# Kernel optimization log

Measured on AMD Instinct MI355X. Metric: run time of the kernel, lower is better.

The kernel has to match this reference:

```python
import jax, jax.numpy as jnp
import numpy as np

EPS = 1e-5
LOSS_WEIGHT = 0.3
IGNORE_INDEX = -100


def rmsnorm(x, w):
    # x: (B,S,D), w: (D,)
    var = jnp.mean(x * x, axis=-1, keepdims=True)
    return x * jax.lax.rsqrt(var + EPS) * w


def cross_entropy(logits, targets):
    # logits: (B,T,V), targets: (B,T) int; ignore_index=-100, mean reduction
    logp = jax.nn.log_softmax(logits, axis=-1)
    valid = targets != IGNORE_INDEX
    safe_t = jnp.where(valid, targets, 0)
    nll = -jnp.take_along_axis(logp, safe_t[..., None], axis=-1)[..., 0]
    nll = jnp.where(valid, nll, 0.0)
    return jnp.sum(nll) / jnp.maximum(jnp.sum(valid), 1)


def setup_inputs() -> dict:
    key = jax.random.key(0)
    ks = jax.random.split(key, 5)
    B, S, D, V, H = 1, 2048, 1024, 50257, 3
    hidden = jax.random.normal(ks[0], (B, S, D), dtype=jnp.float32)
    targets = jax.random.randint(ks[1], (B, S), 0, V, dtype=jnp.int64)
    emb_w = jax.random.normal(ks[2], (V, D), dtype=jnp.float32) * 0.02
    main_norm_w = jnp.ones((D,), dtype=jnp.float32)
    aux_proj_w = jax.random.normal(ks[3], (H - 1, D, D), dtype=jnp.float32) * 0.02
    aux_norm_w = jnp.ones((H - 1, D), dtype=jnp.float32)
    aux_out_w = jax.random.normal(ks[4], (H - 1, V, D), dtype=jnp.float32) * 0.02
    return {"hidden": hidden, "targets": targets, "emb_w": emb_w,
            "main_norm_w": main_norm_w, "aux_proj_w": aux_proj_w,
            "aux_norm_w": aux_norm_w, "aux_out_w": aux_out_w}


def reference(hidden, targets, emb_w, main_norm_w, aux_proj_w, aux_norm_w, aux_out_w):
    # Main head: norm -> tied vocab projection
    main_logits = jnp.einsum('bsd,vd->bsv', rmsnorm(hidden, main_norm_w), emb_w)
    main_loss = cross_entropy(main_logits[:, :-1, :], targets[:, 1:])

    # Auxiliary heads predict t+2, t+3, ...
    n_aux = aux_proj_w.shape[0]
    aux_losses = []
    for i in range(n_aux):
        k = i + 2
        h = jnp.einsum('bsd,ed->bse', hidden, aux_proj_w[i])  # d_model -> d_model
        logits = jnp.einsum('bsd,vd->bsv', rmsnorm(h, aux_norm_w[i]), aux_out_w[i])
        aux_losses.append(cross_entropy(logits[:, :-k, :], targets[:, k:]))
    total_aux = sum(aux_losses) / len(aux_losses) if aux_losses else jnp.float32(0.0)
    loss = main_loss + LOSS_WEIGHT * total_aux
    return main_logits, loss
```

## Files before the change

### kernel.cpp

```cpp
#include <hip/hip_runtime.h>
#include <hip/hip_bf16.h>


typedef __hip_bfloat16 bf16;
typedef __attribute__((ext_vector_type(8))) short bf16x8;
typedef __attribute__((ext_vector_type(4))) float f32x4;

typedef const __attribute__((address_space(1))) void* gptr_t;
typedef __attribute__((address_space(3))) void* lptr_t;

#define S_LEN   2048
#define DMODEL  1024
#define VOCAB   50257
#define NPADR   50304
#define NT128   393
#define NBLK    6288

__device__ __forceinline__ void gload_lds16(const void* g, void* l) {
  __builtin_amdgcn_global_load_lds((gptr_t)g, (lptr_t)l, 16, 0, 0);
}

__global__ __launch_bounds__(256) void k_cvt(const float* __restrict__ src,
                                             bf16* __restrict__ dst,
                                             long rows_src, long rows_pad) {
  const long total4 = rows_pad << 8;
  for (long i = (long)blockIdx.x * 256 + threadIdx.x; i < total4;
       i += (long)gridDim.x * 256) {
    const long e = i << 2;
    const long row = e >> 10;
    alignas(8) bf16 o[4];
    if (row < rows_src) {
      const float4 v = *(const float4*)(src + e);
      o[0] = __float2bfloat16(v.x); o[1] = __float2bfloat16(v.y);
      o[2] = __float2bfloat16(v.z); o[3] = __float2bfloat16(v.w);
    } else {
      o[0] = o[1] = o[2] = o[3] = __float2bfloat16(0.f);
    }
    *(uint2*)(dst + e) = *(const uint2*)o;
  }
}

__global__ __launch_bounds__(256) void k_rms(const float* __restrict__ x,
                                             const float* __restrict__ w,
                                             bf16* __restrict__ xn) {
  const int row = blockIdx.x;
  const int t = threadIdx.x;
  const float4 v = ((const float4*)(x + (size_t)row * DMODEL))[t];
  float ss = v.x*v.x + v.y*v.y + v.z*v.z + v.w*v.w;
  #pragma unroll
  for (int d = 1; d < 64; d <<= 1) ss += __shfl_xor(ss, d, 64);
  __shared__ float red[4];
  if ((t & 63) == 0) red[t >> 6] = ss;
  __syncthreads();
  const float tot = red[0] + red[1] + red[2] + red[3];
  const float scale = rsqrtf(tot * (1.f / DMODEL) + 1e-5f);
  const float4 wv = ((const float4*)w)[t];
  alignas(8) bf16 o[4];
  o[0] = __float2bfloat16(v.x * scale * wv.x);
  o[1] = __float2bfloat16(v.y * scale * wv.y);
  o[2] = __float2bfloat16(v.z * scale * wv.z);
  o[3] = __float2bfloat16(v.w * scale * wv.w);
  *(uint2*)(xn + (size_t)row * DMODEL + t * 4) = *(const uint2*)o;
}

template<bool WRITE_OUT>
__global__ __launch_bounds__(256, 2)
void k_gemm128(const bf16* __restrict__ A, const bf16* __restrict__ B,
               float* __restrict__ C, long ldc, int Nvalid,
               const int* __restrict__ targets, int shift,
               float* __restrict__ pmax, float* __restrict__ psum,
               float* __restrict__ ptgt, int ntiles) {
  __shared__ bf16 As[2][128 * 32];
  __shared__ bf16 Bs[2][128 * 32];
  __shared__ float lds_m[128][2];
  __shared__ float lds_s[128][2];
  __shared__ int lds_tgt[128];

  const int t = threadIdx.x;
  const int w = t >> 6, l = t & 63, g = l >> 4, q = l & 15;
  const int wr = w >> 1, wc = w & 1;
  const int id = blockIdx.x;
  int bm, bn;
  if (id < 6272) {
    const int x = id & 7, u = id >> 3;
    bm = u & 15;
    bn = x * 49 + (u >> 4);
  } else {
    bm = id - 6272;
    bn = 392;
  }

  f32x4 acc[4][4];
  #pragma unroll
  for (int i = 0; i < 4; ++i)
    #pragma unroll
    for (int j = 0; j < 4; ++j)
      #pragma unroll
      for (int r = 0; r < 4; ++r) acc[i][j][r] = 0.f;

  char* dA = (char*)As + w * 1024;
  char* dB = (char*)Bs + w * 1024;
  const int scol = ((t & 3) * 16) ^ (((t >> 5) & 1) * 32);
  const char* gA0 = (const char*)(A + (size_t)(bm * 128 + (t >> 2)) * DMODEL) + scol;
  const char* gA1 = gA0 + (size_t)64 * DMODEL * 2;
  const char* gB0 = (const char*)(B + (size_t)(bn * 128 + (t >> 2)) * DMODEL) + scol;
  const char* gB1 = gB0 + (size_t)64 * DMODEL * 2;

  const int laneoff = (q * 64 + g * 16) ^ (((q >> 3) & 1) << 5);
  const char* rdA = (const char*)As + wr * 4096 + laneoff;
  const char* rdB = (const char*)Bs + wc * 4096 + laneoff;

  for (int k0 = 0; k0 < 16; ++k0) {
    const int kb = k0 * 128;
    gload_lds16(gA0 + kb, dA);
    gload_lds16(gA1 + kb, dA + 4096);
    gload_lds16(gA0 + kb + 64, dA + 8192);
    gload_lds16(gA1 + kb + 64, dA + 12288);
    gload_lds16(gB0 + kb, dB);
    gload_lds16(gB1 + kb, dB + 4096);
    gload_lds16(gB0 + kb + 64, dB + 8192);
    gload_lds16(gB1 + kb + 64, dB + 12288);
    __syncthreads();
    bf16x8 a[4], b[4];
    #pragma unroll
    for (int mi = 0; mi < 4; ++mi) a[mi] = *(const bf16x8*)(rdA + mi * 1024);
    #pragma unroll
    for (int ni = 0; ni < 4; ++ni) b[ni] = *(const bf16x8*)(rdB + ni * 1024);
    __builtin_amdgcn_s_setprio(1);
    #pragma unroll
    for (int mi = 0; mi < 4; ++mi)
      #pragma unroll
      for (int ni = 0; ni < 4; ++ni)
        acc[mi][ni] = __builtin_amdgcn_mfma_f32_16x16x32_bf16(a[mi], b[ni], acc[mi][ni], 0, 0, 0);
    __builtin_amdgcn_s_setprio(0);
    #pragma unroll
    for (int mi = 0; mi < 4; ++mi) a[mi] = *(const bf16x8*)(rdA + 8192 + mi * 1024);
    #pragma unroll
    for (int ni = 0; ni < 4; ++ni) b[ni] = *(const bf16x8*)(rdB + 8192 + ni * 1024);
    __builtin_amdgcn_s_setprio(1);
    #pragma unroll
    for (int mi = 0; mi < 4; ++mi)
      #pragma unroll
      for (int ni = 0; ni < 4; ++ni)
        acc[mi][ni] = __builtin_amdgcn_mfma_f32_16x16x32_bf16(a[mi], b[ni], acc[mi][ni], 0, 0, 0);
    __builtin_amdgcn_s_setprio(0);
    __syncthreads();
  }

  if constexpr (WRITE_OUT) {
    #pragma unroll
    for (int mi = 0; mi < 4; ++mi) {
      #pragma unroll
      for (int r = 0; r < 4; ++r) {
        const long row = bm * 128 + wr * 64 + mi * 16 + g * 4 + r;
        #pragma unroll
        for (int ni = 0; ni < 4; ++ni) {
          const int col = bn * 128 + wc * 64 + ni * 16 + q;
          if (col < Nvalid)
            __builtin_nontemporal_store(acc[mi][ni][r], &C[row * ldc + col]);
        }
      }
    }
  }

  if (t < 128) {
    const int rowg = bm * 128 + t;
    lds_tgt[t] = (rowg < S_LEN - shift) ? targets[rowg + shift] : -1;
  }
  __syncthreads();
  #pragma unroll
  for (int mi = 0; mi < 4; ++mi) {
    #pragma unroll
    for (int r = 0; r < 4; ++r) {
      const int rl = wr * 64 + mi * 16 + g * 4 + r;
      const int tgt = lds_tgt[rl];
      float v[4];
      #pragma unroll
      for (int ni = 0; ni < 4; ++ni) {
        const int n = bn * 128 + wc * 64 + ni * 16 + q;
        const float av = acc[mi][ni][r];
        if (n == tgt) ptgt[bm * 128 + rl] = av;
        v[ni] = (n < Nvalid) ? av : -1e30f;
      }
      float m = fmaxf(fmaxf(v[0], v[1]), fmaxf(v[2], v[3]));
      #pragma unroll
      for (int d = 1; d < 16; d <<= 1) m = fmaxf(m, __shfl_xor(m, d, 64));
      float s = 0.f;
      #pragma unroll
      for (int ni = 0; ni < 4; ++ni) s += __expf(v[ni] - m);
      #pragma unroll
      for (int d = 1; d < 16; d <<= 1) s += __shfl_xor(s, d, 64);
      if (q == 0) { lds_m[rl][wc] = m; lds_s[rl][wc] = s; }
    }
  }
  __syncthreads();
  if (t < 128) {
    const float m0 = lds_m[t][0], m1 = lds_m[t][1];
    const float s0 = lds_s[t][0], s1 = lds_s[t][1];
    const float M = fmaxf(m0, m1);
    const float Ssum = s0 * __expf(m0 - M) + s1 * __expf(m1 - M);
    const size_t idx = (size_t)(bm * 128 + t) * ntiles + bn;
    pmax[idx] = M;
    psum[idx] = Ssum;
  }
}

__global__ __launch_bounds__(256, 2)
void k_gemm(const bf16* __restrict__ A, const bf16* __restrict__ B,
            float* __restrict__ C, long ldc, int Nvalid) {
  constexpr int K = DMODEL;
  __shared__ bf16 As[128 * 32];
  __shared__ bf16 Bs[128 * 32];

  const int t = threadIdx.x;
  const int bn = blockIdx.x, bm = blockIdx.y;
  const int w = t >> 6, l = t & 63, g = l >> 4, q = l & 15;
  const int wr = w >> 1, wc = w & 1;

  f32x4 acc[4][4];
  #pragma unroll
  for (int i = 0; i < 4; ++i)
    #pragma unroll
    for (int j = 0; j < 4; ++j)
      #pragma unroll
      for (int r = 0; r < 4; ++r) acc[i][j][r] = 0.f;

  char* lA0 = (char*)As + w * 1024;
  char* lA1 = (char*)As + 4096 + w * 1024;
  char* lB0 = (char*)Bs + w * 1024;
  char* lB1 = (char*)Bs + 4096 + w * 1024;
  const char* gA0 = (const char*)(A + (size_t)(bm * 128 + (t >> 2)) * K) + (t & 3) * 16;
  const char* gA1 = gA0 + (size_t)64 * K * 2;
  const char* gB0 = (const char*)(B + (size_t)(bn * 128 + (t >> 2)) * K) + (t & 3) * 16;
  const char* gB1 = gB0 + (size_t)64 * K * 2;

  for (int k0 = 0; k0 < K; k0 += 32) {
    const int kb = k0 * 2;
    gload_lds16(gA0 + kb, lA0);
    gload_lds16(gA1 + kb, lA1);
    gload_lds16(gB0 + kb, lB0);
    gload_lds16(gB1 + kb, lB1);
    __syncthreads();
    bf16x8 a[4], b[4];
    #pragma unroll
    for (int mi = 0; mi < 4; ++mi)
      a[mi] = *(const bf16x8*)&As[(wr * 64 + mi * 16 + q) * 32 + g * 8];
    #pragma unroll
    for (int ni = 0; ni < 4; ++ni)
      b[ni] = *(const bf16x8*)&Bs[(wc * 64 + ni * 16 + q) * 32 + g * 8];
    #pragma unroll
    for (int mi = 0; mi < 4; ++mi)
      #pragma unroll
      for (int ni = 0; ni < 4; ++ni)
        acc[mi][ni] = __builtin_amdgcn_mfma_f32_16x16x32_bf16(a[mi], b[ni], acc[mi][ni], 0, 0, 0);
    __syncthreads();
  }

  #pragma unroll
  for (int mi = 0; mi < 4; ++mi) {
    #pragma unroll
    for (int r = 0; r < 4; ++r) {
      const long row = bm * 128 + wr * 64 + mi * 16 + g * 4 + r;
      #pragma unroll
      for (int ni = 0; ni < 4; ++ni) {
        const int col = bn * 128 + wc * 64 + ni * 16 + q;
        if (col < Nvalid) C[row * ldc + col] = acc[mi][ni][r];
      }
    }
  }
}

__global__ __launch_bounds__(64) void k_combine(const float* __restrict__ pmax,
                                                const float* __restrict__ psum,
                                                const float* __restrict__ ptgt,
                                                float* __restrict__ nll,
                                                int ntiles, int nv) {
  const int r = blockIdx.x;
  const int l = threadIdx.x;
  float M = -1e30f, Ssum = 0.f;
  for (int tl = l; tl < ntiles; tl += 64) {
    const float m = pmax[(size_t)r * ntiles + tl];
    const float s = psum[(size_t)r * ntiles + tl];
    const float nM = fmaxf(M, m);
    Ssum = Ssum * __expf(M - nM) + s * __expf(m - nM);
    M = nM;
  }
  #pragma unroll
  for (int d = 1; d < 64; d <<= 1) {
    const float m2 = __shfl_xor(M, d, 64);
    const float s2 = __shfl_xor(Ssum, d, 64);
    const float nM = fmaxf(M, m2);
    Ssum = Ssum * __expf(M - nM) + s2 * __expf(m2 - nM);
    M = nM;
  }
  if (l == 0) nll[r] = (r < nv) ? (M + logf(Ssum) - ptgt[r]) : 0.f;
}

__global__ __launch_bounds__(256) void k_loss(const float* __restrict__ nll,
                                              float* __restrict__ out) {
  __shared__ float sh[256];
  const int t = threadIdx.x;
  float sums[3];
  #pragma unroll
  for (int h = 0; h < 3; ++h) {
    const int nv = 2047 - h;
    float s = 0.f;
    for (int r = t; r < nv; r += 256) s += nll[h * 2048 + r];
    sh[t] = s; __syncthreads();
    for (int off = 128; off > 0; off >>= 1) {
      if (t < off) sh[t] += sh[t + off];
      __syncthreads();
    }
    sums[h] = sh[0]; __syncthreads();
  }
  if (t == 0)
    out[0] = sums[0] / 2047.f + 0.3f * 0.5f * (sums[1] / 2046.f + sums[2] / 2045.f);
}

extern "C" void kernel_launch(void* const* d_in, const int* in_sizes, int n_in,
                              void* d_out, int out_size, void* d_ws, size_t ws_size,
                              hipStream_t stream) {
  const float* hidden      = (const float*)d_in[0];
  const int*   targets     = (const int*)d_in[1];
  const float* emb_w       = (const float*)d_in[2];
  const float* main_norm_w = (const float*)d_in[3];
  const float* aux_proj_w  = (const float*)d_in[4];
  const float* aux_norm_w  = (const float*)d_in[5];
  const float* aux_out_w   = (const float*)d_in[6];
  float* out = (float*)d_out;

  char* ws = (char*)d_ws;
  bf16*  Wb    = (bf16*)(ws);
  bf16*  hb    = (bf16*)(ws + 104857600);
  bf16*  xn    = (bf16*)(ws + 109051904);
  bf16*  projb = (bf16*)(ws + 113246208);
  float* hbuf  = (float*)(ws + 117440512);
  float* pmax  = (float*)(ws + 125829120);
  float* psum  = (float*)(ws + 129105920);
  float* ptgt  = (float*)(ws + 132382720);
  float* nll   = (float*)(ws + 132390912);

  k_cvt<<<2048, 256, 0, stream>>>(hidden, hb, 2048, 2048);
  k_cvt<<<2048, 256, 0, stream>>>(aux_proj_w, projb, 2048, 2048);
  k_rms<<<2048, 256, 0, stream>>>(hidden, main_norm_w, xn);

  k_cvt<<<2048, 256, 0, stream>>>(emb_w, Wb, VOCAB, NPADR);
  k_gemm128<true><<<NBLK, 256, 0, stream>>>(
      xn, Wb, out, VOCAB, VOCAB, targets, 1, pmax, psum, ptgt, NT128);
  k_combine<<<2048, 64, 0, stream>>>(pmax, psum, ptgt, nll, NT128, 2047);

  for (int i = 0; i < 2; ++i) {
    k_cvt<<<2048, 256, 0, stream>>>(aux_out_w + (size_t)i * VOCAB * DMODEL, Wb, VOCAB, NPADR);
    k_gemm<<<dim3(8, 16), 256, 0, stream>>>(
        hb, projb + (size_t)i * DMODEL * DMODEL, hbuf, DMODEL, DMODEL);
    k_rms<<<2048, 256, 0, stream>>>(hbuf, aux_norm_w + (size_t)i * DMODEL, xn);
    k_gemm128<false><<<NBLK, 256, 0, stream>>>(
        xn, Wb, nullptr, 0, VOCAB, targets, i + 2, pmax, psum, ptgt, NT128);
    k_combine<<<2048, 64, 0, stream>>>(pmax, psum, ptgt, nll + (i + 1) * 2048, NT128, 2048 - (i + 2));
  }

  k_loss<<<1, 256, 0, stream>>>(nll, out + (size_t)S_LEN * VOCAB);
}
```

Baseline: 1.029 ms.

## Fuse fp32-to-bf16 weight conversion into vocab GEMM B-tile loading

```diff
diff --git a/kernel.cpp b/kernel.cpp
--- a/kernel.cpp
+++ b/kernel.cpp
@@ -12,7 +12,6 @@
 #define S_LEN   2048
 #define DMODEL  1024
 #define VOCAB   50257
-#define NPADR   50304
 #define NT128   393
 #define NBLK    6288
 
@@ -65,7 +64,7 @@
 
 template<bool WRITE_OUT>
 __global__ __launch_bounds__(256, 2)
-void k_gemm128(const bf16* __restrict__ A, const bf16* __restrict__ B,
+void k_gemm128(const bf16* __restrict__ A, const float* __restrict__ Bf,
                float* __restrict__ C, long ldc, int Nvalid,
                const int* __restrict__ targets, int shift,
                float* __restrict__ pmax, float* __restrict__ psum,
@@ -99,28 +98,64 @@
       for (int r = 0; r < 4; ++r) acc[i][j][r] = 0.f;
 
   char* dA = (char*)As + w * 1024;
-  char* dB = (char*)Bs + w * 1024;
   const int scol = ((t & 3) * 16) ^ (((t >> 5) & 1) * 32);
   const char* gA0 = (const char*)(A + (size_t)(bm * 128 + (t >> 2)) * DMODEL) + scol;
   const char* gA1 = gA0 + (size_t)64 * DMODEL * 2;
-  const char* gB0 = (const char*)(B + (size_t)(bn * 128 + (t >> 2)) * DMODEL) + scol;
-  const char* gB1 = gB0 + (size_t)64 * DMODEL * 2;
+
+  const int r_ = t & 127;
+  const int h_ = t >> 7;
+  int brow = bn * 128 + r_;
+  if (brow > VOCAB - 1) brow = VOCAB - 1;
+  const char* gBf = (const char*)(Bf + (size_t)brow * DMODEL + h_ * 32);
+  const int rr_ = r_ & 15;
+  char* wB = (char*)Bs + h_ * 8192 + (r_ >> 4) * 1024 + rr_ * 64;
+  const int xorb = ((rr_ >> 3) & 1) << 5;
+  const int rot = (r_ >> 1) & 3;
+  int boff[4];
+  #pragma unroll
+  for (int j = 0; j < 4; ++j) boff[j] = ((j + rot) & 3) * 32;
 
   const int laneoff = (q * 64 + g * 16) ^ (((q >> 3) & 1) << 5);
   const char* rdA = (const char*)As + wr * 4096 + laneoff;
   const char* rdB = (const char*)Bs + wc * 4096 + laneoff;
 
+  float4 bv0[4], bv1[4];
+  #pragma unroll
+  for (int j = 0; j < 4; ++j) {
+    bv0[j] = *(const float4*)(gBf + boff[j]);
+    bv1[j] = *(const float4*)(gBf + boff[j] + 16);
+  }
+
+  #pragma unroll
   for (int k0 = 0; k0 < 16; ++k0) {
     const int kb = k0 * 128;
     gload_lds16(gA0 + kb, dA);
     gload_lds16(gA1 + kb, dA + 4096);
     gload_lds16(gA0 + kb + 64, dA + 8192);
     gload_lds16(gA1 + kb + 64, dA + 12288);
-    gload_lds16(gB0 + kb, dB);
-    gload_lds16(gB1 + kb, dB + 4096);
-    gload_lds16(gB0 + kb + 64, dB + 8192);
-    gload_lds16(gB1 + kb + 64, dB + 12288);
-    __syncthreads();
+    asm volatile("s_waitcnt vmcnt(4)" ::: "memory");
+    #pragma unroll
+    for (int j = 0; j < 4; ++j) {
+      alignas(16) bf16 c8[8];
+      c8[0] = __float2bfloat16(bv0[j].x); c8[1] = __float2bfloat16(bv0[j].y);
+      c8[2] = __float2bfloat16(bv0[j].z); c8[3] = __float2bfloat16(bv0[j].w);
+      c8[4] = __float2bfloat16(bv1[j].x); c8[5] = __float2bfloat16(bv1[j].y);
+      c8[6] = __float2bfloat16(bv1[j].z); c8[7] = __float2bfloat16(bv1[j].w);
+      *(bf16x8*)(wB + ((boff[j] >> 1) ^ xorb)) = *(const bf16x8*)c8;
+    }
+    if (k0 < 15) {
+      const int nb = (k0 + 1) * 256;
+      #pragma unroll
+      for (int j = 0; j < 4; ++j) {
+        bv0[j] = *(const float4*)(gBf + nb + boff[j]);
+        bv1[j] = *(const float4*)(gBf + nb + boff[j] + 16);
+      }
+      asm volatile("s_waitcnt vmcnt(8) lgkmcnt(0)" ::: "memory");
+    } else {
+      asm volatile("s_waitcnt vmcnt(0) lgkmcnt(0)" ::: "memory");
+    }
+    __builtin_amdgcn_s_barrier();
+
     bf16x8 a[4], b[4];
     #pragma unroll
     for (int mi = 0; mi < 4; ++mi) a[mi] = *(const bf16x8*)(rdA + mi * 1024);
@@ -144,7 +179,7 @@
       for (int ni = 0; ni < 4; ++ni)
         acc[mi][ni] = __builtin_amdgcn_mfma_f32_16x16x32_bf16(a[mi], b[ni], acc[mi][ni], 0, 0, 0);
     __builtin_amdgcn_s_setprio(0);
-    __syncthreads();
+    __builtin_amdgcn_s_barrier();
   }
 
   if constexpr (WRITE_OUT) {
@@ -330,32 +365,30 @@
   float* out = (float*)d_out;
 
   char* ws = (char*)d_ws;
-  bf16*  Wb    = (bf16*)(ws);
-  bf16*  hb    = (bf16*)(ws + 104857600);
-  bf16*  xn    = (bf16*)(ws + 109051904);
-  bf16*  projb = (bf16*)(ws + 113246208);
-  float* hbuf  = (float*)(ws + 117440512);
-  float* pmax  = (float*)(ws + 125829120);
-  float* psum  = (float*)(ws + 129105920);
-  float* ptgt  = (float*)(ws + 132382720);
-  float* nll   = (float*)(ws + 132390912);
+  bf16*  hb    = (bf16*)(ws);
+  bf16*  xn    = (bf16*)(ws + 4194304);
+  bf16*  projb = (bf16*)(ws + 8388608);
+  float* hbuf  = (float*)(ws + 12582912);
+  float* pmax  = (float*)(ws + 20971520);
+  float* psum  = (float*)(ws + 24248320);
+  float* ptgt  = (float*)(ws + 27525120);
+  float* nll   = (float*)(ws + 27533312);
 
   k_cvt<<<2048, 256, 0, stream>>>(hidden, hb, 2048, 2048);
   k_cvt<<<2048, 256, 0, stream>>>(aux_proj_w, projb, 2048, 2048);
   k_rms<<<2048, 256, 0, stream>>>(hidden, main_norm_w, xn);
 
-  k_cvt<<<2048, 256, 0, stream>>>(emb_w, Wb, VOCAB, NPADR);
   k_gemm128<true><<<NBLK, 256, 0, stream>>>(
-      xn, Wb, out, VOCAB, VOCAB, targets, 1, pmax, psum, ptgt, NT128);
+      xn, emb_w, out, VOCAB, VOCAB, targets, 1, pmax, psum, ptgt, NT128);
   k_combine<<<2048, 64, 0, stream>>>(pmax, psum, ptgt, nll, NT128, 2047);
 
   for (int i = 0; i < 2; ++i) {
-    k_cvt<<<2048, 256, 0, stream>>>(aux_out_w + (size_t)i * VOCAB * DMODEL, Wb, VOCAB, NPADR);
     k_gemm<<<dim3(8, 16), 256, 0, stream>>>(
         hb, projb + (size_t)i * DMODEL * DMODEL, hbuf, DMODEL, DMODEL);
     k_rms<<<2048, 256, 0, stream>>>(hbuf, aux_norm_w + (size_t)i * DMODEL, xn);
     k_gemm128<false><<<NBLK, 256, 0, stream>>>(
-        xn, Wb, nullptr, 0, VOCAB, targets, i + 2, pmax, psum, ptgt, NT128);
+        xn, aux_out_w + (size_t)i * VOCAB * DMODEL, nullptr, 0, VOCAB,
+        targets, i + 2, pmax, psum, ptgt, NT128);
     k_combine<<<2048, 64, 0, stream>>>(pmax, psum, ptgt, nll + (i + 1) * 2048, NT128, 2048 - (i + 2));
   }
 
```

After: 1.358 ms. +31.9%, slower.
